# Kernel optimization log

Hardware: AMD Instinct MI355X
Metric: run time of the kernel (lower is better)

Reference implementation:

```python
import jax, jax.numpy as jnp
import numpy as np

TOPK = 6
ROUTE_SCALE = 1.5


def setup_inputs() -> dict:
    key = jax.random.key(0)
    k1, k2, k3 = jax.random.split(key, 3)
    N, D, E = 16384, 4096, 256
    x = jax.random.normal(k1, (N, D), dtype=jnp.float32)
    weight = jax.random.normal(k2, (E, D), dtype=jnp.float32) * (D ** -0.5)
    bias = jax.random.normal(k3, (E,), dtype=jnp.float32) * 0.02
    return {"x": x, "weight": weight, "bias": bias}


def reference(x, weight, bias):
    # gate linear: [N, D] @ [E, D]^T -> [N, E], computed in fp32
    scores = jnp.einsum('nd,ed->ne', x.astype(jnp.float32), weight.astype(jnp.float32))
    # sqrtsoftplus score function
    original_scores = jnp.sqrt(jax.nn.softplus(scores))
    # bias only affects expert selection, not the routing weights
    biased = original_scores + bias
    _, indices = jax.lax.top_k(biased, TOPK)          # [N, TOPK] int32
    weights = jnp.take_along_axis(original_scores, indices, axis=-1)
    # non-softmax score func -> renormalize selected weights
    weights = weights / jnp.sum(weights, axis=-1, keepdims=True)
    weights = weights * ROUTE_SCALE
    return weights, indices
```

## Files before the change

kernel.cpp:

```cpp
#include <hip/hip_runtime.h>
#include <math.h>

constexpr int D     = 4096;
constexpr int D4    = 1024;
constexpr int E     = 256;
constexpr int TK    = 6;
constexpr int BM    = 64;
constexpr int NT    = 512;
constexpr int NTILE = 128;
constexpr float TAU = 3e-5f;

typedef __attribute__((ext_vector_type(8)))  short short8;
typedef __attribute__((ext_vector_type(16))) float float16;
typedef unsigned short ushort_t;

#define GAS __attribute__((address_space(1)))
#define LAS __attribute__((address_space(3)))

__device__ __forceinline__ ushort_t f2bf(float f) {
  unsigned u = __float_as_uint(f);
  return (ushort_t)((u + 0x7fffu + ((u >> 16) & 1u)) >> 16);
}
__device__ __forceinline__ float bf2f(ushort_t h) {
  return __uint_as_float(((unsigned)h) << 16);
}
__device__ __forceinline__ int swz4(int r) { return (r & 3) ^ ((r >> 2) & 3); }

__device__ __forceinline__ void gload_lds16(const ushort_t* g, ushort_t* l) {
  __builtin_amdgcn_global_load_lds((const GAS unsigned int*)g,
                                   (LAS unsigned int*)l, 16, 0, 0);
}

struct __align__(16) SMem {
  union {
    struct {
      ushort_t Bh[2][E * 32];
      ushort_t Bl[2][E * 32];
      ushort_t Ah[2][BM * 32];
      ushort_t Al[2][BM * 32];
    } st;
    struct {
      float val[BM * 33];
      int   id [BM * 33];
    } mg;
  } u;
  float  bias[E];
  int    nflag;
  int    flagrow[BM];
  int    flagid[BM][8];
  double exact[8];
};

__global__ __launch_bounds__(256)
void conv_w(const float* __restrict__ wg, ushort_t* __restrict__ whi,
            ushort_t* __restrict__ wlo)
{
  size_t i = (size_t)blockIdx.x * 256 + threadIdx.x;
  float4 v = ((const float4*)wg)[i];
  float a[4] = {v.x, v.y, v.z, v.w};
  ushort_t h[4], l[4];
#pragma unroll
  for (int j = 0; j < 4; ++j) {
    h[j] = f2bf(a[j]);
    l[j] = f2bf(a[j] - bf2f(h[j]));
  }
  *(uint2*)&whi[i * 4] = *(uint2*)h;
  *(uint2*)&wlo[i * 4] = *(uint2*)l;
}

__global__ __launch_bounds__(NT, 2)
void gate_kernel(const float* __restrict__ xg, const float* __restrict__ wg,
                 const float* __restrict__ bg,
                 const ushort_t* __restrict__ whi, const ushort_t* __restrict__ wlo,
                 float* __restrict__ outw, float* __restrict__ outi)
{
  __shared__ SMem sm;
  const int t    = threadIdx.x;
  const int row0 = blockIdx.x * BM;
  const int wv   = t >> 6;
  const int lane = t & 63;
  const int rb   = wv & 1;
  const int eg   = wv >> 1;

  if (t < E) sm.bias[t] = bg[t];
  if (t == 0) sm.nflag = 0;

  const float4* x4 = (const float4*)xg;
  const float4* w4 = (const float4*)wg;

  float16 acc0, acc1;
#pragma unroll
  for (int i = 0; i < 16; ++i) { acc0[i] = 0.f; acc1[i] = 0.f; }

  const int a_row = t >> 3;
  const int a_c   = t & 7;
  float4 xP;

  const int be_rel = lane >> 2;
  const int bchunk = lane & 3;

  auto load_x = [&](int kt) {
    xP = x4[(size_t)(row0 + a_row) * D4 + kt * 8 + a_c];
  };
  auto stage_B = [&](int kt, int p) {
    const int k0 = kt * 32;
#pragma unroll
    for (int j = 0; j < 2; ++j) {
      const int e  = wv * 32 + j * 16 + be_rel;
      const int cs = bchunk ^ swz4(e);
      const size_t go = (size_t)e * D + k0 + cs * 8;
      gload_lds16(whi + go, &sm.u.st.Bh[p][(wv * 32 + j * 16) * 32]);
      gload_lds16(wlo + go, &sm.u.st.Bl[p][(wv * 32 + j * 16) * 32]);
    }
  };
  auto store_A = [&](int p) {
    float av[4] = {xP.x, xP.y, xP.z, xP.w};
    ushort_t h[4], l[4];
#pragma unroll
    for (int i = 0; i < 4; ++i) {
      h[i] = f2bf(av[i]);
      l[i] = f2bf(av[i] - bf2f(h[i]));
    }
    const int c  = a_c >> 1, hh = a_c & 1;
    const int sl = (c ^ swz4(a_row)) * 8 + hh * 4;
    *(uint2*)&sm.u.st.Ah[p][a_row * 32 + sl] = *(uint2*)h;
    *(uint2*)&sm.u.st.Al[p][a_row * 32 + sl] = *(uint2*)l;
  };

  const int m  = lane & 31;
  const int hf = lane >> 5;
  const int sA    = swz4(m);
  const int aRow  = (rb * 32 + m) * 32;
  const int b0Row = (eg * 64 + m) * 32;
  const int b1Row = (eg * 64 + 32 + m) * 32;

  load_x(0);
  stage_B(0, 0);
  store_A(0);
  load_x(1);
  __syncthreads();

  for (int kt = 0; kt < NTILE; ++kt) {
    const int p = kt & 1;
    if (kt + 1 < NTILE) {
      stage_B(kt + 1, p ^ 1);
      store_A(p ^ 1);
      if (kt + 2 < NTILE) load_x(kt + 2);
    }
#pragma unroll
    for (int ks = 0; ks < 2; ++ks) {
      const int sl = ((2 * ks + hf) ^ sA) * 8;
      short8 ahi = *(const short8*)&sm.u.st.Ah[p][aRow + sl];
      short8 alo = *(const short8*)&sm.u.st.Al[p][aRow + sl];
      short8 b0h = *(const short8*)&sm.u.st.Bh[p][b0Row + sl];
      short8 b0l = *(const short8*)&sm.u.st.Bl[p][b0Row + sl];
      short8 b1h = *(const short8*)&sm.u.st.Bh[p][b1Row + sl];
      short8 b1l = *(const short8*)&sm.u.st.Bl[p][b1Row + sl];
      acc0 = __builtin_amdgcn_mfma_f32_32x32x16_bf16(ahi, b0h, acc0, 0, 0, 0);
      acc0 = __builtin_amdgcn_mfma_f32_32x32x16_bf16(ahi, b0l, acc0, 0, 0, 0);
      acc0 = __builtin_amdgcn_mfma_f32_32x32x16_bf16(alo, b0h, acc0, 0, 0, 0);
      acc1 = __builtin_amdgcn_mfma_f32_32x32x16_bf16(ahi, b1h, acc1, 0, 0, 0);
      acc1 = __builtin_amdgcn_mfma_f32_32x32x16_bf16(ahi, b1l, acc1, 0, 0, 0);
      acc1 = __builtin_amdgcn_mfma_f32_32x32x16_bf16(alo, b1h, acc1, 0, 0, 0);
    }
    __syncthreads();
  }

  const int e0id = eg * 64 + m;
  const int e1id = eg * 64 + 32 + m;
  const float bia0 = sm.bias[e0id];
  const float bia1 = sm.bias[e1id];

#pragma unroll
  for (int reg = 0; reg < 16; ++reg) {
    const int row_local = rb * 32 + (reg & 3) + 8 * (reg >> 2) + 4 * hf;
    float s0 = acc0[reg], s1 = acc1[reg];
    float v0 = sqrtf(fmaxf(s0, 0.f) + log1pf(expf(-fabsf(s0)))) + bia0;
    float v1 = sqrtf(fmaxf(s1, 0.f) + log1pf(expf(-fabsf(s1)))) + bia1;
    float tv[8]; int ti[8];
#pragma unroll
    for (int s = 0; s < 8; ++s) {
      float bv; int bi;
      if (v0 >= v1) { bv = v0; bi = e0id; } else { bv = v1; bi = e1id; }
#pragma unroll
      for (int off = 1; off < 32; off <<= 1) {
        float ov = __shfl_xor(bv, off, 64);
        int   oi = __shfl_xor(bi, off, 64);
        if (ov > bv || (ov == bv && oi < bi)) { bv = ov; bi = oi; }
      }
      tv[s] = bv; ti[s] = bi;
      if (bi == e0id) v0 = -INFINITY;
      else if (bi == e1id) v1 = -INFINITY;
    }
    if (m == 0) {
#pragma unroll
      for (int s = 0; s < 8; ++s) {
        sm.u.mg.val[row_local * 33 + eg * 8 + s] = tv[s];
        sm.u.mg.id [row_local * 33 + eg * 8 + s] = ti[s];
      }
    }
  }
  __syncthreads();

  {
    const int r = t >> 3, g = t & 7;
    float mv[4]; int mi[4];
#pragma unroll
    for (int q = 0; q < 4; ++q) {
      mv[q] = sm.u.mg.val[r * 33 + q * 8 + g];
      mi[q] = sm.u.mg.id [r * 33 + q * 8 + g];
    }
    float tv[8]; int ti[8];
#pragma unroll
    for (int s = 0; s < 8; ++s) {
      float bv = mv[0]; int bi = mi[0];
#pragma unroll
      for (int q = 1; q < 4; ++q)
        if (mv[q] > bv || (mv[q] == bv && mi[q] < bi)) { bv = mv[q]; bi = mi[q]; }
#pragma unroll
      for (int off = 1; off < 8; off <<= 1) {
        float ov = __shfl_xor(bv, off, 64);
        int   oi = __shfl_xor(bi, off, 64);
        if (ov > bv || (ov == bv && oi < bi)) { bv = ov; bi = oi; }
      }
      tv[s] = bv; ti[s] = bi;
#pragma unroll
      for (int q = 0; q < 4; ++q)
        if (mi[q] == bi) mv[q] = -INFINITY;
    }
    if (g == 0) {
      bool flag = false;
#pragma unroll
      for (int i = 0; i < 7; ++i) flag |= (tv[i] - tv[i + 1] < TAU);
      const int grow = row0 + r;
      if (!flag) {
        float og[6], ssum = 0.f;
#pragma unroll
        for (int i = 0; i < 6; ++i) { og[i] = tv[i] - sm.bias[ti[i]]; ssum += og[i]; }
        const float sc = 1.5f / ssum;
#pragma unroll
        for (int i = 0; i < 6; ++i) {
          outw[(size_t)grow * TK + i] = og[i] * sc;
          outi[(size_t)grow * TK + i] = (float)ti[i];
        }
      } else {
        int slot = atomicAdd(&sm.nflag, 1);
        sm.flagrow[slot] = grow;
#pragma unroll
        for (int i = 0; i < 8; ++i) sm.flagid[slot][i] = ti[i];
      }
    }
  }
  __syncthreads();

  const int nf = sm.nflag;
  for (int f = 0; f < nf; ++f) {
    const int grow = sm.flagrow[f];
    const int e    = sm.flagid[f][wv];
    double accd = 0.0;
    const float4* xr = x4 + (size_t)grow * D4 + lane * 16;
    const float4* wr = w4 + (size_t)e    * D4 + lane * 16;
#pragma unroll
    for (int i = 0; i < 16; ++i) {
      float4 xv = xr[i], wl = wr[i];
      accd = fma((double)xv.x, (double)wl.x, accd);
      accd = fma((double)xv.y, (double)wl.y, accd);
      accd = fma((double)xv.z, (double)wl.z, accd);
      accd = fma((double)xv.w, (double)wl.w, accd);
    }
#pragma unroll
    for (int off = 1; off < 64; off <<= 1)
      accd += __shfl_xor(accd, off, 64);
    if (lane == 0) {
      double sp = fmax(accd, 0.0) + log1p(exp(-fabs(accd)));
      sm.exact[wv] = sqrt(sp);
    }
    __syncthreads();
    if (t == 0) {
      double ov[8]; int oid[8], ordr[8];
      for (int i = 0; i < 8; ++i) { ov[i] = sm.exact[i]; oid[i] = sm.flagid[f][i]; ordr[i] = i; }
      for (int i = 0; i < 6; ++i) {
        int b = i;
        for (int j = i + 1; j < 8; ++j) {
          double bj = ov[ordr[j]] + (double)sm.bias[oid[ordr[j]]];
          double bb = ov[ordr[b]] + (double)sm.bias[oid[ordr[b]]];
          if (bj > bb || (bj == bb && oid[ordr[j]] < oid[ordr[b]])) b = j;
        }
        int tmp = ordr[i]; ordr[i] = ordr[b]; ordr[b] = tmp;
      }
      double ssum = 0.0;
      for (int i = 0; i < 6; ++i) ssum += ov[ordr[i]];
      double sc = 1.5 / ssum;
      for (int i = 0; i < 6; ++i) {
        outw[(size_t)grow * TK + i] = (float)(ov[ordr[i]] * sc);
        outi[(size_t)grow * TK + i] = (float)oid[ordr[i]];
      }
    }
    __syncthreads();
  }
}

extern "C" void kernel_launch(void* const* d_in, const int* in_sizes, int n_in,
                              void* d_out, int out_size, void* d_ws, size_t ws_size,
                              hipStream_t stream) {
  const float* x = (const float*)d_in[0];
  const float* w = (const float*)d_in[1];
  const float* b = (const float*)d_in[2];
  float* out  = (float*)d_out;
  const int N = in_sizes[0] / D;

  ushort_t* whi = (ushort_t*)d_ws;
  ushort_t* wlo = whi + (size_t)E * D;

  float* outw = out;
  float* outi = out + (size_t)N * TK;

  hipLaunchKernelGGL(conv_w, dim3(E * D / 4 / 256), dim3(256), 0, stream,
                     w, whi, wlo);
  hipLaunchKernelGGL(gate_kernel, dim3(N / BM), dim3(NT), 0, stream,
                     x, w, b, whi, wlo, outw, outi);
}
```

Baseline: 565.5 us.

## Deepen B staging to four-stage pipeline and re-split waves across expert columns

Reorganizes the GEMM so each wave owns a 32-expert slice across all 64 rows, with B staged in a 4-deep LDS ring and x prefetched three tiles ahead. Manual vmcnt/lgkmcnt waits and raw s_barrier replace __syncthreads so global-to-LDS loads overlap further with MFMA work. The top-k per wave switches to a max-shuffle plus ballot winner selection, and the merge now combines 8 partial lists per row instead of 4. It uses more LDS per block, which may limit occupancy, and depends on hand-counted wait counts being right.

```diff
diff --git a/kernel.cpp b/kernel.cpp
--- a/kernel.cpp
+++ b/kernel.cpp
@@ -34,14 +34,14 @@
 struct __align__(16) SMem {
   union {
     struct {
-      ushort_t Bh[2][E * 32];
-      ushort_t Bl[2][E * 32];
+      ushort_t Bh[4][8][32 * 32];
+      ushort_t Bl[4][8][32 * 32];
       ushort_t Ah[2][BM * 32];
       ushort_t Al[2][BM * 32];
     } st;
     struct {
-      float val[BM * 33];
-      int   id [BM * 33];
+      float val[BM * 65];
+      int   id [BM * 65];
     } mg;
   } u;
   float  bias[E];
@@ -50,6 +50,7 @@
   int    flagid[BM][8];
   double exact[8];
 };
+static_assert(sizeof(SMem) <= 160 * 1024, "LDS overflow");
 
 __global__ __launch_bounds__(256)
 void conv_w(const float* __restrict__ wg, ushort_t* __restrict__ whi,
@@ -67,6 +68,11 @@
   *(uint2*)&whi[i * 4] = *(uint2*)h;
   *(uint2*)&wlo[i * 4] = *(uint2*)l;
 }
+
+#define WAITV5   asm volatile("s_waitcnt vmcnt(5)" ::: "memory")
+#define WAITV0   asm volatile("s_waitcnt vmcnt(0)" ::: "memory")
+#define LGKM0    asm volatile("s_waitcnt lgkmcnt(0)" ::: "memory")
+#define MEMFENCE asm volatile("" ::: "memory")
 
 __global__ __launch_bounds__(NT, 2)
 void gate_kernel(const float* __restrict__ xg, const float* __restrict__ wg,
@@ -79,8 +85,8 @@
   const int row0 = blockIdx.x * BM;
   const int wv   = t >> 6;
   const int lane = t & 63;
-  const int rb   = wv & 1;
-  const int eg   = wv >> 1;
+  const int m    = lane & 31;
+  const int hf   = lane >> 5;
 
   if (t < E) sm.bias[t] = bg[t];
   if (t == 0) sm.nflag = 0;
@@ -94,27 +100,24 @@
 
   const int a_row = t >> 3;
   const int a_c   = t & 7;
-  float4 xP;
-
-  const int be_rel = lane >> 2;
-  const int bchunk = lane & 3;
-
-  auto load_x = [&](int kt) {
-    xP = x4[(size_t)(row0 + a_row) * D4 + kt * 8 + a_c];
+
+  const int e16 = lane >> 2;
+  const int ch  = lane & 3;
+
+  const int sA = swz4(m);
+
+  auto stage_B = [&](int kt, int p) {
+#pragma unroll
+    for (int j = 0; j < 2; ++j) {
+      const int er = j * 16 + e16;
+      const int cs = ch ^ swz4(er);
+      const size_t go = (size_t)(wv * 32 + er) * D + kt * 32 + cs * 8;
+      gload_lds16(whi + go, &sm.u.st.Bh[p][wv][j * 512]);
+      gload_lds16(wlo + go, &sm.u.st.Bl[p][wv][j * 512]);
+    }
   };
-  auto stage_B = [&](int kt, int p) {
-    const int k0 = kt * 32;
-#pragma unroll
-    for (int j = 0; j < 2; ++j) {
-      const int e  = wv * 32 + j * 16 + be_rel;
-      const int cs = bchunk ^ swz4(e);
-      const size_t go = (size_t)e * D + k0 + cs * 8;
-      gload_lds16(whi + go, &sm.u.st.Bh[p][(wv * 32 + j * 16) * 32]);
-      gload_lds16(wlo + go, &sm.u.st.Bl[p][(wv * 32 + j * 16) * 32]);
-    }
-  };
-  auto store_A = [&](int p) {
-    float av[4] = {xP.x, xP.y, xP.z, xP.w};
+  auto store_A = [&](int p, float4 xv) {
+    float av[4] = {xv.x, xv.y, xv.z, xv.w};
     ushort_t h[4], l[4];
 #pragma unroll
     for (int i = 0; i < 4; ++i) {
@@ -126,77 +129,91 @@
     *(uint2*)&sm.u.st.Ah[p][a_row * 32 + sl] = *(uint2*)h;
     *(uint2*)&sm.u.st.Al[p][a_row * 32 + sl] = *(uint2*)l;
   };
-
-  const int m  = lane & 31;
-  const int hf = lane >> 5;
-  const int sA    = swz4(m);
-  const int aRow  = (rb * 32 + m) * 32;
-  const int b0Row = (eg * 64 + m) * 32;
-  const int b1Row = (eg * 64 + 32 + m) * 32;
-
-  load_x(0);
-  stage_B(0, 0);
-  store_A(0);
-  load_x(1);
-  __syncthreads();
-
-  for (int kt = 0; kt < NTILE; ++kt) {
-    const int p = kt & 1;
-    if (kt + 1 < NTILE) {
-      stage_B(kt + 1, p ^ 1);
-      store_A(p ^ 1);
-      if (kt + 2 < NTILE) load_x(kt + 2);
-    }
+  auto compute = [&](int pa, int pb) {
 #pragma unroll
     for (int ks = 0; ks < 2; ++ks) {
       const int sl = ((2 * ks + hf) ^ sA) * 8;
-      short8 ahi = *(const short8*)&sm.u.st.Ah[p][aRow + sl];
-      short8 alo = *(const short8*)&sm.u.st.Al[p][aRow + sl];
-      short8 b0h = *(const short8*)&sm.u.st.Bh[p][b0Row + sl];
-      short8 b0l = *(const short8*)&sm.u.st.Bl[p][b0Row + sl];
-      short8 b1h = *(const short8*)&sm.u.st.Bh[p][b1Row + sl];
-      short8 b1l = *(const short8*)&sm.u.st.Bl[p][b1Row + sl];
-      acc0 = __builtin_amdgcn_mfma_f32_32x32x16_bf16(ahi, b0h, acc0, 0, 0, 0);
-      acc0 = __builtin_amdgcn_mfma_f32_32x32x16_bf16(ahi, b0l, acc0, 0, 0, 0);
-      acc0 = __builtin_amdgcn_mfma_f32_32x32x16_bf16(alo, b0h, acc0, 0, 0, 0);
-      acc1 = __builtin_amdgcn_mfma_f32_32x32x16_bf16(ahi, b1h, acc1, 0, 0, 0);
-      acc1 = __builtin_amdgcn_mfma_f32_32x32x16_bf16(ahi, b1l, acc1, 0, 0, 0);
-      acc1 = __builtin_amdgcn_mfma_f32_32x32x16_bf16(alo, b1h, acc1, 0, 0, 0);
-    }
-    __syncthreads();
-  }
-
-  const int e0id = eg * 64 + m;
-  const int e1id = eg * 64 + 32 + m;
-  const float bia0 = sm.bias[e0id];
-  const float bia1 = sm.bias[e1id];
-
-#pragma unroll
-  for (int reg = 0; reg < 16; ++reg) {
-    const int row_local = rb * 32 + (reg & 3) + 8 * (reg >> 2) + 4 * hf;
-    float s0 = acc0[reg], s1 = acc1[reg];
-    float v0 = sqrtf(fmaxf(s0, 0.f) + log1pf(expf(-fabsf(s0)))) + bia0;
-    float v1 = sqrtf(fmaxf(s1, 0.f) + log1pf(expf(-fabsf(s1)))) + bia1;
-    float tv[8]; int ti[8];
-#pragma unroll
-    for (int s = 0; s < 8; ++s) {
-      float bv; int bi;
-      if (v0 >= v1) { bv = v0; bi = e0id; } else { bv = v1; bi = e1id; }
-#pragma unroll
-      for (int off = 1; off < 32; off <<= 1) {
-        float ov = __shfl_xor(bv, off, 64);
-        int   oi = __shfl_xor(bi, off, 64);
-        if (ov > bv || (ov == bv && oi < bi)) { bv = ov; bi = oi; }
-      }
-      tv[s] = bv; ti[s] = bi;
-      if (bi == e0id) v0 = -INFINITY;
-      else if (bi == e1id) v1 = -INFINITY;
-    }
-    if (m == 0) {
-#pragma unroll
-      for (int s = 0; s < 8; ++s) {
-        sm.u.mg.val[row_local * 33 + eg * 8 + s] = tv[s];
-        sm.u.mg.id [row_local * 33 + eg * 8 + s] = ti[s];
+      short8 a0h = *(const short8*)&sm.u.st.Ah[pa][m * 32 + sl];
+      short8 a0l = *(const short8*)&sm.u.st.Al[pa][m * 32 + sl];
+      short8 a1h = *(const short8*)&sm.u.st.Ah[pa][(32 + m) * 32 + sl];
+      short8 a1l = *(const short8*)&sm.u.st.Al[pa][(32 + m) * 32 + sl];
+      short8 bh  = *(const short8*)&sm.u.st.Bh[pb][wv][m * 32 + sl];
+      short8 bl  = *(const short8*)&sm.u.st.Bl[pb][wv][m * 32 + sl];
+      acc0 = __builtin_amdgcn_mfma_f32_32x32x16_bf16(a0h, bh, acc0, 0, 0, 0);
+      acc0 = __builtin_amdgcn_mfma_f32_32x32x16_bf16(a0h, bl, acc0, 0, 0, 0);
+      acc0 = __builtin_amdgcn_mfma_f32_32x32x16_bf16(a0l, bh, acc0, 0, 0, 0);
+      acc1 = __builtin_amdgcn_mfma_f32_32x32x16_bf16(a1h, bh, acc1, 0, 0, 0);
+      acc1 = __builtin_amdgcn_mfma_f32_32x32x16_bf16(a1h, bl, acc1, 0, 0, 0);
+      acc1 = __builtin_amdgcn_mfma_f32_32x32x16_bf16(a1l, bh, acc1, 0, 0, 0);
+    }
+  };
+
+  float4 x0 = x4[(size_t)(row0 + a_row) * D4 + 0 * 8 + a_c];
+  float4 xA = x4[(size_t)(row0 + a_row) * D4 + 1 * 8 + a_c];
+  stage_B(0, 0);
+  WAITV5;
+  store_A(0, x0);
+  float4 xB = x4[(size_t)(row0 + a_row) * D4 + 2 * 8 + a_c];
+  stage_B(1, 1);
+  LGKM0;
+  __builtin_amdgcn_s_barrier();
+  MEMFENCE;
+
+#define TILE_BODY(KT, XS)                                                     \
+  do {                                                                        \
+    const int P   = (KT) & 3;                                                 \
+    const int PW  = ((KT) + 2) & 3;                                           \
+    const int PA  = (KT) & 1;                                                 \
+    const int PA1 = ((KT) + 1) & 1;                                           \
+    WAITV5;                                  \
+    store_A(PA1, XS);                                                         \
+    { const int kl = ((KT) + 3 < NTILE) ? (KT) + 3 : NTILE - 1;               \
+      XS = x4[(size_t)(row0 + a_row) * D4 + kl * 8 + a_c]; }                  \
+    { const int kb = ((KT) + 2 < NTILE) ? (KT) + 2 : NTILE - 1;               \
+      stage_B(kb, PW); }                                                      \
+    compute(PA, P);                                                           \
+    LGKM0;                          \
+    __builtin_amdgcn_s_barrier();                                             \
+    MEMFENCE;                                                                 \
+  } while (0)
+
+  for (int it = 0; it < NTILE / 4; ++it) {
+    const int kt = it * 4;
+    TILE_BODY(kt + 0, xA);
+    TILE_BODY(kt + 1, xB);
+    TILE_BODY(kt + 2, xA);
+    TILE_BODY(kt + 3, xB);
+  }
+#undef TILE_BODY
+
+  WAITV0;
+  __syncthreads();
+
+  const int eBase  = wv * 32;
+  const int myE    = eBase + m;
+  const float myBias = sm.bias[myE];
+
+#pragma unroll
+  for (int b = 0; b < 2; ++b) {
+#pragma unroll
+    for (int reg = 0; reg < 16; ++reg) {
+      const int row_local = b * 32 + (reg & 3) + 8 * (reg >> 2) + 4 * hf;
+      float s = b ? acc1[reg] : acc0[reg];
+      float v = sqrtf(fmaxf(s, 0.f) + log1pf(expf(-fabsf(s)))) + myBias;
+#pragma unroll
+      for (int ssel = 0; ssel < 8; ++ssel) {
+        float bv = v;
+#pragma unroll
+        for (int off = 1; off < 32; off <<= 1)
+          bv = fmaxf(bv, __shfl_xor(bv, off, 64));
+        unsigned long long ball = __ballot(v == bv);
+        unsigned hm = (unsigned)(ball >> (hf * 32));
+        int mwin = __ffs(hm) - 1;
+        if (m == mwin) {
+          sm.u.mg.val[row_local * 65 + wv * 8 + ssel] = v;
+          sm.u.mg.id [row_local * 65 + wv * 8 + ssel] = myE;
+          v = -INFINITY;
+        }
       }
     }
   }
@@ -204,18 +221,18 @@
 
   {
     const int r = t >> 3, g = t & 7;
-    float mv[4]; int mi[4];
-#pragma unroll
-    for (int q = 0; q < 4; ++q) {
-      mv[q] = sm.u.mg.val[r * 33 + q * 8 + g];
-      mi[q] = sm.u.mg.id [r * 33 + q * 8 + g];
+    float mv[8]; int mi[8];
+#pragma unroll
+    for (int q = 0; q < 8; ++q) {
+      mv[q] = sm.u.mg.val[r * 65 + q * 8 + g];
+      mi[q] = sm.u.mg.id [r * 65 + q * 8 + g];
     }
     float tv[8]; int ti[8];
 #pragma unroll
     for (int s = 0; s < 8; ++s) {
       float bv = mv[0]; int bi = mi[0];
 #pragma unroll
-      for (int q = 1; q < 4; ++q)
+      for (int q = 1; q < 8; ++q)
         if (mv[q] > bv || (mv[q] == bv && mi[q] < bi)) { bv = mv[q]; bi = mi[q]; }
 #pragma unroll
       for (int off = 1; off < 8; off <<= 1) {
@@ -225,7 +242,7 @@
       }
       tv[s] = bv; ti[s] = bi;
 #pragma unroll
-      for (int q = 0; q < 4; ++q)
+      for (int q = 0; q < 8; ++q)
         if (mi[q] == bi) mv[q] = -INFINITY;
     }
     if (g == 0) {
```

After: 561.8 us. Within noise of the previous version (-0.6%).
